# Performance work log

Measured on AMD Instinct MI355X. Metric: run time of the kernel, lower is better.

The kernel has to match this reference:

```python
import jax, jax.numpy as jnp
import numpy as np

C = 128
HID = 4 * C
K = 7
PAD = K // 2
B, T, F = 4, 512, 128
LN_EPS = 1e-5
LS_INIT = 1e-2  # LayerScale init value


def setup_inputs() -> dict:
    key = jax.random.key(0)
    ks = jax.random.split(key, 4)
    x = jax.random.normal(ks[0], (B, C, T, F), dtype=jnp.float32)
    dw_w = jax.random.normal(ks[1], (C, 1, K, K), dtype=jnp.float32) * (1.0 / K)
    dw_b = jnp.zeros((C,), dtype=jnp.float32)
    ln_g = jnp.ones((C,), dtype=jnp.float32)
    ln_b = jnp.zeros((C,), dtype=jnp.float32)
    w1 = jax.random.normal(ks[2], (HID, C), dtype=jnp.float32) * (1.0 / np.sqrt(C))
    b1 = jnp.zeros((HID,), dtype=jnp.float32)
    w2 = jax.random.normal(ks[3], (C, HID), dtype=jnp.float32) * (1.0 / np.sqrt(HID))
    b2 = jnp.zeros((C,), dtype=jnp.float32)
    ls = jnp.full((C,), LS_INIT, dtype=jnp.float32)
    return {"x": x, "dw_w": dw_w, "dw_b": dw_b, "ln_g": ln_g, "ln_b": ln_b,
            "w1": w1, "b1": b1, "w2": w2, "b2": b2, "ls": ls}


def reference(x, dw_w, dw_b, ln_g, ln_b, w1, b1, w2, b2, ls):
    # depthwise 2D conv over (T, F), groups = C
    y = jax.lax.conv_general_dilated(
        x, dw_w, window_strides=(1, 1), padding=[(PAD, PAD), (PAD, PAD)],
        feature_group_count=x.shape[1],
        dimension_numbers=("NCHW", "OIHW", "NCHW"))
    y = y + dw_b[None, :, None, None]
    # channels-last for LayerNorm over C and pointwise MLP
    y = jnp.transpose(y, (0, 2, 3, 1))  # [B, T, F, C]
    mu = jnp.mean(y, axis=-1, keepdims=True)
    var = jnp.mean(jnp.square(y - mu), axis=-1, keepdims=True)
    y = (y - mu) * jax.lax.rsqrt(var + LN_EPS) * ln_g + ln_b
    # pointwise MLP: C -> 4C -> GELU -> C
    h = jax.nn.gelu(jnp.einsum("btfc,hc->btfh", y, w1) + b1)
    y = jnp.einsum("btfh,ch->btfc", h, w2) + b2
    # LayerScale: per-channel multiply
    y = y * ls
    return jnp.transpose(y, (0, 3, 1, 2))  # back to [B, C, T, F]
```

## Files before the change

### kernel.cpp

```cpp
#include <hip/hip_runtime.h>
#include <hip/hip_bf16.h>
#include <math.h>

typedef __bf16 bf16x8 __attribute__((ext_vector_type(8)));
typedef float f32x4 __attribute__((ext_vector_type(4)));
typedef unsigned int u32x4 __attribute__((ext_vector_type(4)));

constexpr int C_ = 128, HID_ = 512, T_ = 512, F_ = 128, B_ = 4;
constexpr int PIMG = T_ * F_;

__global__ void wcvt_k(const float* __restrict__ w1, const float* __restrict__ w2,
                       __bf16* __restrict__ w1b, __bf16* __restrict__ w2b) {
    int i = blockIdx.x * 256 + threadIdx.x;
    w1b[i] = (__bf16)w1[i];
    w2b[i] = (__bf16)w2[i];
}

template <typename OT>
__global__ __launch_bounds__(256) void dwconv_k(
    const float* __restrict__ x, const float* __restrict__ dww,
    const float* __restrict__ dwb, OT* __restrict__ y) {
    __shared__ float tile[38][140];
    const int bx = blockIdx.x;
    const int tt = bx & 15, c = (bx >> 4) & 127, b = bx >> 11;
    const int t0 = tt * 32;
    const float* xp = x + ((size_t)(b * C_ + c)) * PIMG;

    float wr[49];
#pragma unroll
    for (int i = 0; i < 49; ++i) wr[i] = dww[c * 49 + i];
    const float bias = dwb[c];

    const int colq = threadIdx.x & 31;
    const int rg = threadIdx.x >> 5;
    for (int r = rg; r < 38; r += 8) {
        const int t = t0 - 3 + r;
        f32x4 v = {0.f, 0.f, 0.f, 0.f};
        if (t >= 0 && t < T_) v = *(const f32x4*)(xp + (size_t)t * F_ + colq * 4);
        *(f32x4*)&tile[r][4 + colq * 4] = v;
        if (colq == 0) { tile[r][1] = 0.f; tile[r][2] = 0.f; tile[r][3] = 0.f; }
        if (colq == 31) { tile[r][132] = 0.f; tile[r][133] = 0.f; tile[r][134] = 0.f; }
    }
    __syncthreads();

    const int f = threadIdx.x & 127;
    const int g = threadIdx.x >> 7;
    float acc[16];
#pragma unroll
    for (int i = 0; i < 16; ++i) acc[i] = 0.f;
#pragma unroll
    for (int df = 0; df < 7; ++df) {
        float colv[22];
#pragma unroll
        for (int j = 0; j < 22; ++j) colv[j] = tile[g * 16 + j][1 + f + df];
#pragma unroll
        for (int dr = 0; dr < 7; ++dr) {
            const float wv = wr[dr * 7 + df];
#pragma unroll
            for (int i = 0; i < 16; ++i) acc[i] += colv[i + dr] * wv;
        }
    }
    OT* yp = y + ((size_t)(b * C_ + c)) * PIMG + (size_t)(t0 + g * 16) * F_ + f;
#pragma unroll
    for (int i = 0; i < 16; ++i) yp[(size_t)i * F_] = (OT)(acc[i] + bias);
}

__device__ __forceinline__ float gelu_tanh(float xv) {
    float u = 0.7978845608028654f * (xv + 0.044715f * xv * xv * xv);
    u = fminf(fmaxf(u, -15.f), 15.f);
    const float e = __expf(2.f * u);
    const float th = (e - 1.f) / (e + 1.f);
    return 0.5f * xv * (1.f + th);
}

template <typename YT>
__global__ __launch_bounds__(512, 4) void lnmlp_k(
    const YT* y,
    const __bf16* __restrict__ w1b, const __bf16* __restrict__ w2b,
    const float* __restrict__ lng, const float* __restrict__ lnb,
    const float* __restrict__ b1, const float* __restrict__ b2,
    const float* __restrict__ ls, float* out) {
    __shared__ __align__(16) unsigned char smem[66560];
    float (*yraw)[68] = (float (*)[68])smem;
    unsigned short (*yb)[136] = (unsigned short (*)[136])(smem + 34816);
    unsigned short (*hl)[520] = (unsigned short (*)[520])smem;
    __shared__ double pls[8][64], pls2[8][64];
    __shared__ double mud[64], rsd[64];
    __shared__ float lgs[C_], lbs[C_];

    const int tid = threadIdx.x;
    const int lane = tid & 63, wv = tid >> 6;
    const int b = blockIdx.x >> 10;
    const int p0 = (blockIdx.x & 1023) * 64;
    const YT* yp = y + (size_t)b * ((size_t)C_ * PIMG) + p0;

    if (tid < 128) lgs[tid] = lng[tid];
    else if (tid < 256) lbs[tid - 128] = lnb[tid - 128];

    if constexpr (sizeof(YT) == 2) {
#pragma unroll
        for (int it = 0; it < 2; ++it) {
            const int c = it * 64 + (tid >> 3);
            const int seg = (tid & 7) * 8;
            u32x4 raw = *(const u32x4*)(yp + (size_t)c * PIMG + seg);
            bf16x8 v = __builtin_bit_cast(bf16x8, raw);
            f32x4 lo = {(float)v[0], (float)v[1], (float)v[2], (float)v[3]};
            f32x4 hi = {(float)v[4], (float)v[5], (float)v[6], (float)v[7]};
            *(f32x4*)&yraw[c][seg] = lo;
            *(f32x4*)&yraw[c][seg + 4] = hi;
        }
    } else {
#pragma unroll
        for (int it = 0; it < 4; ++it) {
            const int c = it * 32 + (tid >> 4);
            const int ch = (tid & 15) * 4;
            *(f32x4*)&yraw[c][ch] = *(const f32x4*)(yp + (size_t)c * PIMG + ch);
        }
    }
    __syncthreads();

    {
        double s = 0.0, s2 = 0.0;
#pragma unroll
        for (int i = 0; i < 16; ++i) {
            const double v = (double)yraw[wv * 16 + i][lane];
            s += v;
            s2 = fma(v, v, s2);
        }
        pls[wv][lane] = s;
        pls2[wv][lane] = s2;
    }
    __syncthreads();

    if (tid < 64) {
        const int p = tid;
        double s = 0.0, s2 = 0.0;
#pragma unroll
        for (int w = 0; w < 8; ++w) { s += pls[w][p]; s2 += pls2[w][p]; }
        const double mu = s * (1.0 / 128.0);
        const double var = (s2 - s * s * (1.0 / 128.0)) * (1.0 / 128.0);
        mud[p] = mu;
        rsd[p] = 1.0 / sqrt(var + 1e-5);
    }
    __syncthreads();

    {
        const int pos = tid & 63;
        const int cbase = (tid >> 6) * 16;
        const double mu = mud[pos], rs = rsd[pos];
#pragma unroll
        for (int j = 0; j < 16; j += 2) {
            const int c = cbase + j;
            const float v0 = (float)(((double)yraw[c][pos] - mu) * rs) * lgs[c] + lbs[c];
            const float v1 = (float)(((double)yraw[c + 1][pos] - mu) * rs) * lgs[c + 1] + lbs[c + 1];
            *(unsigned int*)&yb[pos][c] =
                (unsigned int)__builtin_bit_cast(unsigned short, (__bf16)v0) |
                ((unsigned int)__builtin_bit_cast(unsigned short, (__bf16)v1) << 16);
        }
    }
    __syncthreads();

    const int l15 = lane & 15, l4 = lane >> 4;

    f32x4 acc1[4][4];
#pragma unroll
    for (int m = 0; m < 4; ++m)
#pragma unroll
        for (int ct = 0; ct < 4; ++ct) acc1[m][ct] = (f32x4){0.f, 0.f, 0.f, 0.f};

    const __bf16* w1p = w1b + (size_t)(wv * 64) * 128;
#pragma unroll
    for (int k0 = 0; k0 < 128; k0 += 32) {
        bf16x8 bh[4];
#pragma unroll
        for (int ct = 0; ct < 4; ++ct)
            bh[ct] = *(const bf16x8*)&yb[ct * 16 + l15][k0 + l4 * 8];
#pragma unroll
        for (int m = 0; m < 4; ++m) {
            bf16x8 ah = *(const bf16x8*)(w1p + (size_t)(m * 16 + l15) * 128 + k0 + l4 * 8);
#pragma unroll
            for (int ct = 0; ct < 4; ++ct)
                acc1[m][ct] = __builtin_amdgcn_mfma_f32_16x16x32_bf16(ah, bh[ct], acc1[m][ct], 0, 0, 0);
        }
    }
    __syncthreads();

#pragma unroll
    for (int m = 0; m < 4; ++m) {
        const int hid0 = wv * 64 + m * 16 + l4 * 4;
        const float bb0 = b1[hid0], bb1 = b1[hid0 + 1], bb2v = b1[hid0 + 2], bb3 = b1[hid0 + 3];
#pragma unroll
        for (int ct = 0; ct < 4; ++ct) {
            const int p = ct * 16 + l15;
            float hv[4];
            hv[0] = gelu_tanh(acc1[m][ct][0] + bb0);
            hv[1] = gelu_tanh(acc1[m][ct][1] + bb1);
            hv[2] = gelu_tanh(acc1[m][ct][2] + bb2v);
            hv[3] = gelu_tanh(acc1[m][ct][3] + bb3);
            unsigned int ph[2];
#pragma unroll
            for (int q = 0; q < 2; ++q) {
                ph[q] = (unsigned int)__builtin_bit_cast(unsigned short, (__bf16)hv[2 * q]) |
                        ((unsigned int)__builtin_bit_cast(unsigned short, (__bf16)hv[2 * q + 1]) << 16);
            }
            *(unsigned long long*)&hl[p][hid0] = (unsigned long long)ph[0] | ((unsigned long long)ph[1] << 32);
        }
    }
    __syncthreads();

    f32x4 acc2[4];
#pragma unroll
    for (int ct = 0; ct < 4; ++ct) acc2[ct] = (f32x4){0.f, 0.f, 0.f, 0.f};

    const __bf16* w2p = w2b + (size_t)(wv * 16) * 512;
#pragma unroll
    for (int k0 = 0; k0 < 512; k0 += 32) {
        bf16x8 bh[4];
#pragma unroll
        for (int ct = 0; ct < 4; ++ct)
            bh[ct] = *(const bf16x8*)&hl[ct * 16 + l15][k0 + l4 * 8];
        bf16x8 ah = *(const bf16x8*)(w2p + (size_t)l15 * 512 + k0 + l4 * 8);
#pragma unroll
        for (int ct = 0; ct < 4; ++ct)
            acc2[ct] = __builtin_amdgcn_mfma_f32_16x16x32_bf16(ah, bh[ct], acc2[ct], 0, 0, 0);
    }

    float* op = out + (size_t)b * ((size_t)C_ * PIMG) + p0;
    {
        const int c0 = wv * 16 + l4 * 4;
        float bv[4], lv[4];
#pragma unroll
        for (int r = 0; r < 4; ++r) { bv[r] = b2[c0 + r]; lv[r] = ls[c0 + r]; }
#pragma unroll
        for (int ct = 0; ct < 4; ++ct) {
            const int p = ct * 16 + l15;
#pragma unroll
            for (int r = 0; r < 4; ++r)
                op[(size_t)(c0 + r) * PIMG + p] = (acc2[ct][r] + bv[r]) * lv[r];
        }
    }
}

extern "C" void kernel_launch(void* const* d_in, const int* in_sizes, int n_in,
                              void* d_out, int out_size, void* d_ws, size_t ws_size,
                              hipStream_t stream) {
    const float* x   = (const float*)d_in[0];
    const float* dww = (const float*)d_in[1];
    const float* dwb = (const float*)d_in[2];
    const float* lng = (const float*)d_in[3];
    const float* lnb = (const float*)d_in[4];
    const float* w1  = (const float*)d_in[5];
    const float* b1  = (const float*)d_in[6];
    const float* w2  = (const float*)d_in[7];
    const float* b2  = (const float*)d_in[8];
    const float* ls  = (const float*)d_in[9];
    float* out = (float*)d_out;

    __bf16* w1b = (__bf16*)d_ws;
    __bf16* w2b = w1b + 65536;
    wcvt_k<<<65536 / 256, 256, 0, stream>>>(w1, w2, w1b, w2b);

    const size_t interElems = (size_t)B_ * C_ * PIMG;
    const size_t needWs = 262144 + interElems * 2;
    if (ws_size >= needWs) {
        __bf16* yc = (__bf16*)((char*)d_ws + 262144);
        dwconv_k<__bf16><<<B_ * C_ * (T_ / 32), 256, 0, stream>>>(x, dww, dwb, yc);
        lnmlp_k<__bf16><<<B_ * (PIMG / 64), 512, 0, stream>>>(yc, w1b, w2b,
                                                              lng, lnb, b1, b2, ls, out);
    } else {
        float* yc = out;
        dwconv_k<float><<<B_ * C_ * (T_ / 32), 256, 0, stream>>>(x, dww, dwb, yc);
        lnmlp_k<float><<<B_ * (PIMG / 64), 512, 0, stream>>>(yc, w1b, w2b,
                                                             lng, lnb, b1, b2, ls, out);
    }
}
```

Measured before the change: 279.5 us.

## Shrink LDS footprint in LN+MLP kernel to raise occupancy

Reduces the fused LayerNorm+MLP kernel's shared memory by staging bf16 inputs as bf16 via direct global-to-LDS loads and splitting the hidden activation buffer into two halves written and consumed in sequence. Launch bounds are raised to allow six blocks per CU. GELU is rewritten in the equivalent sigmoid form with a fast divide to cut ALU work. The halved hidden buffer adds two extra barriers and keeps GELU outputs in registers, which may increase register pressure under the tighter occupancy bound.

```diff
diff --git a/kernel.cpp b/kernel.cpp
--- a/kernel.cpp
+++ b/kernel.cpp
@@ -4,7 +4,6 @@
 
 typedef __bf16 bf16x8 __attribute__((ext_vector_type(8)));
 typedef float f32x4 __attribute__((ext_vector_type(4)));
-typedef unsigned int u32x4 __attribute__((ext_vector_type(4)));
 
 constexpr int C_ = 128, HID_ = 512, T_ = 512, F_ = 128, B_ = 4;
 constexpr int PIMG = T_ * F_;
@@ -66,24 +65,26 @@
 }
 
 __device__ __forceinline__ float gelu_tanh(float xv) {
-    float u = 0.7978845608028654f * (xv + 0.044715f * xv * xv * xv);
-    u = fminf(fmaxf(u, -15.f), 15.f);
-    const float e = __expf(2.f * u);
-    const float th = (e - 1.f) / (e + 1.f);
-    return 0.5f * xv * (1.f + th);
+    const float u2 = 1.5957691216057308f * (xv + 0.044715f * xv * xv * xv);
+    const float e = __expf(-u2);
+    return __fdividef(xv, 1.f + e);
 }
 
 template <typename YT>
-__global__ __launch_bounds__(512, 4) void lnmlp_k(
+__global__ __launch_bounds__(512, 6) void lnmlp_k(
     const YT* y,
     const __bf16* __restrict__ w1b, const __bf16* __restrict__ w2b,
     const float* __restrict__ lng, const float* __restrict__ lnb,
     const float* __restrict__ b1, const float* __restrict__ b2,
     const float* __restrict__ ls, float* out) {
-    __shared__ __align__(16) unsigned char smem[66560];
-    float (*yraw)[68] = (float (*)[68])smem;
-    unsigned short (*yb)[136] = (unsigned short (*)[136])(smem + 34816);
-    unsigned short (*hl)[520] = (unsigned short (*)[520])smem;
+    constexpr bool YBF = (sizeof(YT) == 2);
+    constexpr int YRAW_BYTES = YBF ? 16384 : 34816;
+    constexpr int SMEM_SZ = YRAW_BYTES + 17408;
+    __shared__ __align__(16) unsigned char smem[SMEM_SZ];
+    unsigned short (*yraw_b)[64] = (unsigned short (*)[64])smem;
+    float (*yraw_f)[68] = (float (*)[68])smem;
+    unsigned short (*yb)[136] = (unsigned short (*)[136])(smem + YRAW_BYTES);
+    unsigned short (*hl)[264] = (unsigned short (*)[264])smem;
     __shared__ double pls[8][64], pls2[8][64];
     __shared__ double mud[64], rsd[64];
     __shared__ float lgs[C_], lbs[C_];
@@ -97,33 +98,34 @@
     if (tid < 128) lgs[tid] = lng[tid];
     else if (tid < 256) lbs[tid - 128] = lnb[tid - 128];
 
-    if constexpr (sizeof(YT) == 2) {
+    if constexpr (YBF) {
 #pragma unroll
         for (int it = 0; it < 2; ++it) {
-            const int c = it * 64 + (tid >> 3);
-            const int seg = (tid & 7) * 8;
-            u32x4 raw = *(const u32x4*)(yp + (size_t)c * PIMG + seg);
-            bf16x8 v = __builtin_bit_cast(bf16x8, raw);
-            f32x4 lo = {(float)v[0], (float)v[1], (float)v[2], (float)v[3]};
-            f32x4 hi = {(float)v[4], (float)v[5], (float)v[6], (float)v[7]};
-            *(f32x4*)&yraw[c][seg] = lo;
-            *(f32x4*)&yraw[c][seg + 4] = hi;
+            const int row0 = it * 64 + wv * 8;
+            const YT* gsrc = yp + (size_t)(row0 + (lane >> 3)) * PIMG + (lane & 7) * 8;
+            __builtin_amdgcn_global_load_lds((const unsigned int*)gsrc,
+                                             (unsigned int*)&yraw_b[row0][0], 16, 0, 0);
         }
     } else {
 #pragma unroll
         for (int it = 0; it < 4; ++it) {
             const int c = it * 32 + (tid >> 4);
             const int ch = (tid & 15) * 4;
-            *(f32x4*)&yraw[c][ch] = *(const f32x4*)(yp + (size_t)c * PIMG + ch);
-        }
-    }
-    __syncthreads();
+            *(f32x4*)&yraw_f[c][ch] = *(const f32x4*)(yp + (size_t)c * PIMG + ch);
+        }
+    }
+    __syncthreads();
+
+    auto ldy = [&](int c, int p) -> float {
+        if constexpr (YBF) return (float)__builtin_bit_cast(__bf16, yraw_b[c][p]);
+        else return yraw_f[c][p];
+    };
 
     {
         double s = 0.0, s2 = 0.0;
 #pragma unroll
         for (int i = 0; i < 16; ++i) {
-            const double v = (double)yraw[wv * 16 + i][lane];
+            const double v = (double)ldy(wv * 16 + i, lane);
             s += v;
             s2 = fma(v, v, s2);
         }
@@ -151,8 +153,8 @@
 #pragma unroll
         for (int j = 0; j < 16; j += 2) {
             const int c = cbase + j;
-            const float v0 = (float)(((double)yraw[c][pos] - mu) * rs) * lgs[c] + lbs[c];
-            const float v1 = (float)(((double)yraw[c + 1][pos] - mu) * rs) * lgs[c + 1] + lbs[c + 1];
+            const float v0 = (float)(((double)ldy(c, pos) - mu) * rs) * lgs[c] + lbs[c];
+            const float v1 = (float)(((double)ldy(c + 1, pos) - mu) * rs) * lgs[c + 1] + lbs[c + 1];
             *(unsigned int*)&yb[pos][c] =
                 (unsigned int)__builtin_bit_cast(unsigned short, (__bf16)v0) |
                 ((unsigned int)__builtin_bit_cast(unsigned short, (__bf16)v1) << 16);
@@ -183,27 +185,24 @@
                 acc1[m][ct] = __builtin_amdgcn_mfma_f32_16x16x32_bf16(ah, bh[ct], acc1[m][ct], 0, 0, 0);
         }
     }
-    __syncthreads();
-
+
+    unsigned long long hreg[4][4];
 #pragma unroll
     for (int m = 0; m < 4; ++m) {
         const int hid0 = wv * 64 + m * 16 + l4 * 4;
         const float bb0 = b1[hid0], bb1 = b1[hid0 + 1], bb2v = b1[hid0 + 2], bb3 = b1[hid0 + 3];
 #pragma unroll
         for (int ct = 0; ct < 4; ++ct) {
-            const int p = ct * 16 + l15;
             float hv[4];
             hv[0] = gelu_tanh(acc1[m][ct][0] + bb0);
             hv[1] = gelu_tanh(acc1[m][ct][1] + bb1);
             hv[2] = gelu_tanh(acc1[m][ct][2] + bb2v);
             hv[3] = gelu_tanh(acc1[m][ct][3] + bb3);
-            unsigned int ph[2];
-#pragma unroll
-            for (int q = 0; q < 2; ++q) {
-                ph[q] = (unsigned int)__builtin_bit_cast(unsigned short, (__bf16)hv[2 * q]) |
-                        ((unsigned int)__builtin_bit_cast(unsigned short, (__bf16)hv[2 * q + 1]) << 16);
-            }
-            *(unsigned long long*)&hl[p][hid0] = (unsigned long long)ph[0] | ((unsigned long long)ph[1] << 32);
+            unsigned int lo = (unsigned int)__builtin_bit_cast(unsigned short, (__bf16)hv[0]) |
+                              ((unsigned int)__builtin_bit_cast(unsigned short, (__bf16)hv[1]) << 16);
+            unsigned int hi = (unsigned int)__builtin_bit_cast(unsigned short, (__bf16)hv[2]) |
+                              ((unsigned int)__builtin_bit_cast(unsigned short, (__bf16)hv[3]) << 16);
+            hreg[m][ct] = (unsigned long long)lo | ((unsigned long long)hi << 32);
         }
     }
     __syncthreads();
@@ -211,14 +210,49 @@
     f32x4 acc2[4];
 #pragma unroll
     for (int ct = 0; ct < 4; ++ct) acc2[ct] = (f32x4){0.f, 0.f, 0.f, 0.f};
-
     const __bf16* w2p = w2b + (size_t)(wv * 16) * 512;
-#pragma unroll
-    for (int k0 = 0; k0 < 512; k0 += 32) {
+
+    if (wv < 4) {
+#pragma unroll
+        for (int m = 0; m < 4; ++m) {
+            const int col = wv * 64 + m * 16 + l4 * 4;
+#pragma unroll
+            for (int ct = 0; ct < 4; ++ct)
+                *(unsigned long long*)&hl[ct * 16 + l15][col] = hreg[m][ct];
+        }
+    }
+    __syncthreads();
+
+#pragma unroll
+    for (int k0 = 0; k0 < 256; k0 += 32) {
         bf16x8 bh[4];
 #pragma unroll
         for (int ct = 0; ct < 4; ++ct)
             bh[ct] = *(const bf16x8*)&hl[ct * 16 + l15][k0 + l4 * 8];
+        bf16x8 ah = *(const bf16x8*)(w2p + (size_t)l15 * 512 + k0 + l4 * 8);
+#pragma unroll
+        for (int ct = 0; ct < 4; ++ct)
+            acc2[ct] = __builtin_amdgcn_mfma_f32_16x16x32_bf16(ah, bh[ct], acc2[ct], 0, 0, 0);
+    }
+    __syncthreads();
+
+    if (wv >= 4) {
+#pragma unroll
+        for (int m = 0; m < 4; ++m) {
+            const int col = (wv - 4) * 64 + m * 16 + l4 * 4;
+#pragma unroll
+            for (int ct = 0; ct < 4; ++ct)
+                *(unsigned long long*)&hl[ct * 16 + l15][col] = hreg[m][ct];
+        }
+    }
+    __syncthreads();
+
+#pragma unroll
+    for (int k0 = 256; k0 < 512; k0 += 32) {
+        bf16x8 bh[4];
+#pragma unroll
+        for (int ct = 0; ct < 4; ++ct)
+            bh[ct] = *(const bf16x8*)&hl[ct * 16 + l15][(k0 - 256) + l4 * 8];
         bf16x8 ah = *(const bf16x8*)(w2p + (size_t)l15 * 512 + k0 + l4 * 8);
 #pragma unroll
         for (int ct = 0; ct < 4; ++ct)
```

Result: slower. 425.2 us (+52.1%).
